# Kernel tuning notes

Hardware: AMD Instinct MI355X
Metric: run time of the kernel (lower is better)

Reference implementation:

```python
import jax, jax.numpy as jnp
import numpy as np

N, E, P = 50000, 800000, 12
C0, H1, H2 = 2, 32, 64


def gcn(x, W, b, src, dst, dinv):
    xw = x @ W                                   # [N, out]
    msg = (dinv[src] * dinv[dst])[:, None] * xw[src]
    agg = jax.ops.segment_sum(msg, dst, num_segments=x.shape[0])
    agg = agg + (dinv * dinv)[:, None] * xw      # self-loop term
    return agg + b


def tgcn_cell(x, H, W, b, Wl, bl, src, dst, dinv):
    # TGCN GRU cell (gates stacked as [z, r, h] along leading dim of W/b/Wl/bl)
    cz = gcn(x, W[0], b[0], src, dst, dinv)
    Z = jax.nn.sigmoid(jnp.concatenate([cz, H], axis=1) @ Wl[0] + bl[0])
    cr = gcn(x, W[1], b[1], src, dst, dinv)
    R = jax.nn.sigmoid(jnp.concatenate([cr, H], axis=1) @ Wl[1] + bl[1])
    ch = gcn(x, W[2], b[2], src, dst, dinv)
    Ht = jnp.tanh(jnp.concatenate([ch, H * R], axis=1) @ Wl[2] + bl[2])
    return Z * H + (1.0 - Z) * Ht


def a3tgcn(X, att, W, b, Wl, bl, src, dst, dinv):
    # X: [N, C, P]; attention-weighted sum of per-period TGCN outputs with H=0
    probs = jax.nn.softmax(att)
    n, out = X.shape[0], W.shape[2]
    H0 = jnp.zeros((n, out), X.dtype)

    def body(acc, inp):
        xp, p = inp
        return acc + p * tgcn_cell(xp, H0, W, b, Wl, bl, src, dst, dinv), None

    acc, _ = jax.lax.scan(body, jnp.zeros((n, out), X.dtype),
                          (jnp.moveaxis(X, 2, 0), probs))
    return acc


def setup_inputs() -> dict:
    key = jax.random.key(0)
    ks = jax.random.split(key, 16)
    s = 0.1
    return {
        "x_1": jax.random.normal(ks[0], (N, C0, P), jnp.float32),
        "edge_index_1": jax.random.randint(ks[1], (2, E), 0, N),
        "x_2": jax.random.normal(ks[2], (8, C0, P), jnp.float32),
        "edge_index_2": jax.random.randint(ks[3], (2, 8), 0, 8),
        # A3TGCN layer 1 (in=C0, out=H1): gates stacked [z, r, h]
        "W1": jax.random.normal(ks[4], (3, C0, H1), jnp.float32) * s,
        "b1": jnp.zeros((3, H1), jnp.float32),
        "Wl1": jax.random.normal(ks[5], (3, 2 * H1, H1), jnp.float32) * s,
        "bl1": jnp.zeros((3, H1), jnp.float32),
        "att1": jax.random.normal(ks[6], (P,), jnp.float32),
        # A3TGCN layer 2 (in=H1+1, out=H2)
        "W2": jax.random.normal(ks[7], (3, H1 + 1, H2), jnp.float32) * s,
        "b2": jnp.zeros((3, H2), jnp.float32),
        "Wl2": jax.random.normal(ks[8], (3, 2 * H2, H2), jnp.float32) * s,
        "bl2": jnp.zeros((3, H2), jnp.float32),
        "att2": jax.random.normal(ks[9], (P,), jnp.float32),
        # MLP head
        "lw1": jax.random.normal(ks[10], (H2, H1), jnp.float32) * s,
        "lb1": jnp.zeros((H1,), jnp.float32),
        "lw2": jax.random.normal(ks[11], (H1, P), jnp.float32) * s,
        "lb2": jnp.zeros((P,), jnp.float32),
    }


def reference(x_1, edge_index_1, x_2, edge_index_2,
              W1, b1, Wl1, bl1, att1,
              W2, b2, Wl2, bl2, att2,
              lw1, lb1, lw2, lb2):
    src, dst = edge_index_1[0], edge_index_1[1]
    n, periods = x_1.shape[0], x_1.shape[2]
    # degree (with self-loop) for symmetric GCN normalization
    deg = jax.ops.segment_sum(jnp.ones(src.shape[0], x_1.dtype), dst,
                              num_segments=n) + 1.0
    dinv = jax.lax.rsqrt(deg)

    time = x_1[:, -1, :]                                        # [N, P]
    h = jax.nn.relu(a3tgcn(x_1, att1, W1, b1, Wl1, bl1, src, dst, dinv))
    h = jnp.concatenate([jnp.repeat(h[:, :, None], periods, axis=2),
                         time[:, None, :]], axis=1)             # [N, H1+1, P]
    h = jax.nn.relu(a3tgcn(h, att2, W2, b2, Wl2, bl2, src, dst, dinv))
    h = jax.nn.relu(h @ lw1 + lb1)
    return h @ lw2 + lb2                                        # [N, P]
```

## Files before the change

kernel.cpp:

```cpp
#include <hip/hip_runtime.h>
#include <hip/hip_bf16.h>
#include <hip/hip_fp16.h>
#include <math.h>


typedef float f4v __attribute__((ext_vector_type(4)));

static __device__ __forceinline__ unsigned short f2bf(float f) {
    unsigned u = __float_as_uint(f);
    unsigned r = (u + 0x7FFFu + ((u >> 16) & 1u)) >> 16;
    return (unsigned short)r;
}
static __device__ __forceinline__ float bf2f(unsigned short u) {
    return __uint_as_float(((unsigned)u) << 16);
}
static __device__ __forceinline__ unsigned short f2h(float f) {
    __half h = __float2half_rn(f);
    return *reinterpret_cast<unsigned short*>(&h);
}
static __device__ __forceinline__ float h2f(unsigned short u) {
    __half h;
    *reinterpret_cast<unsigned short*>(&h) = u;
    return __half2float(h);
}

__global__ void zero_ints(int* __restrict__ a, int n) {
    int i = blockIdx.x * blockDim.x + threadIdx.x;
    if (i < n) a[i] = 0;
}

__global__ void cvt_count(const float* __restrict__ in, unsigned short* __restrict__ outh,
                          int n4, int ncb,
                          const int* __restrict__ dst, int* __restrict__ cnt,
                          int* __restrict__ epos, int E) {
    if ((int)blockIdx.x < ncb) {
        int i = (blockIdx.x * blockDim.x + threadIdx.x) * 4;
        if (i + 3 < n4) {
            f4v v = __builtin_nontemporal_load((const f4v*)(in + i));
            ushort4 u = make_ushort4(f2bf(v.x), f2bf(v.y), f2bf(v.z), f2bf(v.w));
            *(ushort4*)(outh + i) = u;
        } else {
            for (int k = 0; k < 4; ++k)
                if (i + k < n4) outh[i + k] = f2bf(in[i + k]);
        }
    } else {
        int e = (blockIdx.x - ncb) * blockDim.x + threadIdx.x;
        if (e < E) {
            int d = __builtin_nontemporal_load(dst + e);
            int pos = atomicAdd(&cnt[d], 1);
            __builtin_nontemporal_store(pos, epos + e);
        }
    }
}

__global__ __launch_bounds__(256) void scan_blocksum(
    const int* __restrict__ cnt, float* __restrict__ dinv,
    int* __restrict__ bsum, int n) {
    int base = blockIdx.x * 1024 + threadIdx.x * 4;
    int s = 0;
    if (base + 3 < n) {
        int4 v = *(const int4*)(cnt + base);
        dinv[base + 0] = rsqrtf((float)v.x + 1.f);
        dinv[base + 1] = rsqrtf((float)v.y + 1.f);
        dinv[base + 2] = rsqrtf((float)v.z + 1.f);
        dinv[base + 3] = rsqrtf((float)v.w + 1.f);
        s = v.x + v.y + v.z + v.w;
    } else {
        for (int k = 0; k < 4; ++k)
            if (base + k < n) {
                int v = cnt[base + k];
                dinv[base + k] = rsqrtf((float)v + 1.f);
                s += v;
            }
    }
    #pragma unroll
    for (int off = 32; off > 0; off >>= 1) s += __shfl_down(s, off, 64);
    __shared__ int ws[4];
    int lane = threadIdx.x & 63, wid = threadIdx.x >> 6;
    if (lane == 0) ws[wid] = s;
    __syncthreads();
    if (threadIdx.x == 0) bsum[blockIdx.x] = ws[0] + ws[1] + ws[2] + ws[3];
}

__global__ void scan_boffs(const int* __restrict__ bsum, int* __restrict__ boffs,
                           int* __restrict__ rowptr, int nb, int n) {
    int lane = threadIdx.x;
    int carry = 0;
    for (int base = 0; base < nb; base += 64) {
        int i = base + lane;
        int v = (i < nb) ? bsum[i] : 0;
        int orig = v;
        #pragma unroll
        for (int off = 1; off < 64; off <<= 1) {
            int t = __shfl_up(v, off, 64);
            if (lane >= off) v += t;
        }
        if (i < nb) boffs[i] = carry + v - orig;
        carry += __shfl(v, 63, 64);
    }
    if (lane == 0) rowptr[n] = carry;
}

__global__ __launch_bounds__(256) void scan_write(
    const int* __restrict__ cnt, const int* __restrict__ boffs,
    int* __restrict__ rowptr, int n) {
    int base = blockIdx.x * 1024 + threadIdx.x * 4;
    int4 v = make_int4(0, 0, 0, 0);
    if (base + 3 < n) {
        v = *(const int4*)(cnt + base);
    } else {
        if (base + 0 < n) v.x = cnt[base + 0];
        if (base + 1 < n) v.y = cnt[base + 1];
        if (base + 2 < n) v.z = cnt[base + 2];
        if (base + 3 < n) v.w = cnt[base + 3];
    }
    int t0 = v.x, t1 = t0 + v.y, t2 = t1 + v.z, t3 = t2 + v.w;
    int lane = threadIdx.x & 63, wid = threadIdx.x >> 6;
    int sc = t3;
    #pragma unroll
    for (int off = 1; off < 64; off <<= 1) {
        int t = __shfl_up(sc, off, 64);
        if (lane >= off) sc += t;
    }
    __shared__ int ws[4];
    if (lane == 63) ws[wid] = sc;
    __syncthreads();
    int woff = 0;
    for (int w = 0; w < wid; ++w) woff += ws[w];
    int off0 = boffs[blockIdx.x] + woff + sc - t3;
    if (base + 3 < n) {
        *(int4*)(rowptr + base) = make_int4(off0, off0 + t0, off0 + t1, off0 + t2);
    } else {
        if (base + 0 < n) rowptr[base + 0] = off0;
        if (base + 1 < n) rowptr[base + 1] = off0 + t0;
        if (base + 2 < n) rowptr[base + 2] = off0 + t1;
        if (base + 3 < n) rowptr[base + 3] = off0 + t2;
    }
}

__global__ void scatter_edges(const int* __restrict__ src, const int* __restrict__ dst,
                              const int* __restrict__ epos,
                              const float* __restrict__ dinv, const int* __restrict__ rowptr,
                              unsigned* __restrict__ cwp, int E) {
    int e = blockIdx.x * blockDim.x + threadIdx.x;
    if (e >= E) return;
    int s = __builtin_nontemporal_load(src + e);
    int d = __builtin_nontemporal_load(dst + e);
    int pos = __builtin_nontemporal_load(epos + e);
    int idx = rowptr[d] + pos;
    float w = dinv[s] * dinv[d];
    unsigned pk = (unsigned)(unsigned short)s | ((unsigned)f2h(w) << 16);
    __builtin_nontemporal_store(pk, cwp + idx);
}

__global__ __launch_bounds__(256) void prep_kernel(
    const float* __restrict__ W1, const float* __restrict__ b1,
    const float* __restrict__ Wl1, const float* __restrict__ bl1,
    const float* __restrict__ att1,
    const float* __restrict__ W2, const float* __restrict__ b2,
    const float* __restrict__ Wl2, const float* __restrict__ bl2,
    const float* __restrict__ att2, float* __restrict__ small) {
    int tid = threadIdx.x;
    for (int t = tid; t < 192; t += blockDim.x) {
        int which = t >> 5, hh = t & 31;
        int g = (which < 3) ? 0 : 2;
        int kind = which % 3;
        const float* Wl = Wl1 + g * 64 * 32;
        float s = 0.f;
        if (kind < 2) {
            const float* Wr = W1 + g * 2 * 32 + kind * 32;
            for (int k = 0; k < 32; ++k) s += Wr[k] * Wl[k * 32 + hh];
        } else {
            const float* br = b1 + g * 32;
            for (int k = 0; k < 32; ++k) s += br[k] * Wl[k * 32 + hh];
            s += bl1[g * 32 + hh];
        }
        small[t] = s;
    }
    for (int t = tid; t < 4096; t += blockDim.x) {
        int gg = t >> 11;
        int rem = t & 2047;
        int i = rem >> 6, j = rem & 63;
        int g = gg ? 2 : 0;
        const float* Wl = Wl2 + g * 128 * 64;
        const float* Wr = W2 + g * 33 * 64 + i * 64;
        float s = 0.f;
        for (int k = 0; k < 64; ++k) s += Wr[k] * Wl[k * 64 + j];
        small[256 + gg * 2048 + i * 64 + j] = s;
    }
    for (int t = tid; t < 256; t += blockDim.x) {
        int which = t >> 6, j = t & 63;
        int g = (which == 0 || which == 2) ? 0 : 2;
        const float* Wl = Wl2 + g * 128 * 64;
        float s = 0.f;
        if (which < 2) {
            const float* Wr = W2 + g * 33 * 64 + 32 * 64;
            for (int k = 0; k < 64; ++k) s += Wr[k] * Wl[k * 64 + j];
        } else {
            const float* br = b2 + g * 64;
            for (int k = 0; k < 64; ++k) s += br[k] * Wl[k * 64 + j];
            s += bl2[g * 64 + j];
        }
        small[4352 + which * 64 + j] = s;
    }
    if (tid == 0) {
        float mx = att1[0];
        for (int p = 1; p < 12; ++p) mx = fmaxf(mx, att1[p]);
        float e[12], sm = 0.f;
        for (int p = 0; p < 12; ++p) { e[p] = expf(att1[p] - mx); sm += e[p]; }
        for (int p = 0; p < 12; ++p) small[192 + p] = e[p] / sm;
        mx = att2[0];
        for (int p = 1; p < 12; ++p) mx = fmaxf(mx, att2[p]);
        sm = 0.f;
        for (int p = 0; p < 12; ++p) { e[p] = expf(att2[p] - mx); sm += e[p]; }
        for (int p = 0; p < 12; ++p) small[4608 + p] = e[p] / sm;
    }
}

__global__ __launch_bounds__(256) void agg1_layer1(
    const float* __restrict__ X, const unsigned short* __restrict__ Xh,
    const int* __restrict__ rowptr, const unsigned* __restrict__ cwp,
    const float* __restrict__ dinv, const float* __restrict__ small,
    unsigned short* __restrict__ hout, float* __restrict__ atime, int n) {
    int lane = threadIdx.x & 31;
    int node = (blockIdx.x * blockDim.x + threadIdx.x) >> 5;
    if (node >= n) return;
    int beg = rowptr[node], end = rowptr[node + 1];
    float acc = 0.f;
    if (lane < 24) {
        float dn = dinv[node];
        acc = dn * dn * __builtin_nontemporal_load(X + (size_t)node * 24 + lane);
        float a0 = 0.f, a1 = 0.f, a2 = 0.f, a3 = 0.f;
        int j = beg;
        for (; j + 4 <= end; j += 4) {
            unsigned c0 = __builtin_nontemporal_load(cwp + j);
            unsigned c1 = __builtin_nontemporal_load(cwp + j + 1);
            unsigned c2 = __builtin_nontemporal_load(cwp + j + 2);
            unsigned c3 = __builtin_nontemporal_load(cwp + j + 3);
            a0 = fmaf(h2f(c0 >> 16), bf2f(Xh[(c0 & 0xFFFFu) * 24 + lane]), a0);
            a1 = fmaf(h2f(c1 >> 16), bf2f(Xh[(c1 & 0xFFFFu) * 24 + lane]), a1);
            a2 = fmaf(h2f(c2 >> 16), bf2f(Xh[(c2 & 0xFFFFu) * 24 + lane]), a2);
            a3 = fmaf(h2f(c3 >> 16), bf2f(Xh[(c3 & 0xFFFFu) * 24 + lane]), a3);
        }
        for (; j < end; ++j) {
            unsigned c = __builtin_nontemporal_load(cwp + j);
            acc = fmaf(h2f(c >> 16), bf2f(Xh[(c & 0xFFFFu) * 24 + lane]), acc);
        }
        acc += (a0 + a1) + (a2 + a3);
    }
    if (lane >= 12 && lane < 24)
        __builtin_nontemporal_store(acc, atime + (size_t)node * 12 + lane - 12);
    float a0z = small[lane], a1z = small[32 + lane], c1z = small[64 + lane];
    float a0h = small[96 + lane], a1h = small[128 + lane], c1h = small[160 + lane];
    float hs = 0.f;
    #pragma unroll
    for (int p = 0; p < 12; ++p) {
        float x0 = __shfl(acc, p, 32);
        float x1 = __shfl(acc, 12 + p, 32);
        float z = 1.f / (1.f + __expf(-fmaf(x0, a0z, fmaf(x1, a1z, c1z))));
        float ht = tanhf(fmaf(x0, a0h, fmaf(x1, a1h, c1h)));
        hs = fmaf(small[192 + p] * (1.f - z), ht, hs);
    }
    hout[(size_t)node * 32 + lane] = f2bf(fmaxf(hs, 0.f));
}

__global__ __launch_bounds__(512, 8) void agg2_layer2(
    const unsigned short* __restrict__ hbuf, const float* __restrict__ atime,
    const int* __restrict__ rowptr, const unsigned* __restrict__ cwp,
    const float* __restrict__ dinv, const float* __restrict__ small,
    const float* __restrict__ lw1, const float* __restrict__ lb1,
    const float* __restrict__ lw2, const float* __restrict__ lb2,
    float* __restrict__ out, int n) {
    __shared__ __align__(16) float4 wqs[1024];
    __shared__ __align__(16) float s_lw1[2048];
    __shared__ float s_pr[16];
    __shared__ __align__(16) float4 scr[8][16];

    for (int t = threadIdx.x; t < 4096; t += 512) {
        int s = t & 3, j = (t >> 2) & 63, k2 = t >> 8;
        int k = 2 * k2 + (s >> 1), zh = s & 1;
        ((float*)wqs)[t] = small[256 + zh * 2048 + k * 64 + j];
    }
    for (int t = threadIdx.x; t < 2048; t += 512) s_lw1[t] = lw1[t];
    if (threadIdx.x < 16) s_pr[threadIdx.x] = (threadIdx.x < 12) ? small[4608 + threadIdx.x] : 0.f;
    __syncthreads();

    int lane = threadIdx.x & 63;
    int wid = threadIdx.x >> 6;
    int ch = lane & 31, half = lane >> 5;
    float qz = small[4352 + lane], qh = small[4416 + lane];
    float czv = small[4480 + lane], chv = small[4544 + lane];
    float lb1v = lb1[ch];
    int p_ = lane & 15, q_ = lane >> 4;
    float lb2v = (q_ == 0 && p_ < 12) ? lb2[p_] : 0.f;
    float wlw2[8];
    #pragma unroll
    for (int i = 0; i < 8; ++i)
        wlw2[i] = (p_ < 12) ? lw2[(q_ * 8 + i) * 12 + p_] : 0.f;

    int totalw = gridDim.x * 8;
    for (int node = blockIdx.x * 8 + wid; node < n; node += totalw) {
        int beg = rowptr[node], end = rowptr[node + 1];
        float dn = dinv[node];
        float acc = (half == 0) ? dn * dn * bf2f(hbuf[(size_t)node * 32 + ch]) : 0.f;
        float a1 = 0.f, a2 = 0.f, a3 = 0.f;
        int j = beg + half;
        for (; j + 6 < end; j += 8) {
            unsigned c0 = __builtin_nontemporal_load(cwp + j);
            unsigned c1 = __builtin_nontemporal_load(cwp + j + 2);
            unsigned c2 = __builtin_nontemporal_load(cwp + j + 4);
            unsigned c3 = __builtin_nontemporal_load(cwp + j + 6);
            acc = fmaf(h2f(c0 >> 16), bf2f(hbuf[(size_t)(c0 & 0xFFFFu) * 32 + ch]), acc);
            a1  = fmaf(h2f(c1 >> 16), bf2f(hbuf[(size_t)(c1 & 0xFFFFu) * 32 + ch]), a1);
            a2  = fmaf(h2f(c2 >> 16), bf2f(hbuf[(size_t)(c2 & 0xFFFFu) * 32 + ch]), a2);
            a3  = fmaf(h2f(c3 >> 16), bf2f(hbuf[(size_t)(c3 & 0xFFFFu) * 32 + ch]), a3);
        }
        for (; j < end; j += 2) {
            unsigned c = __builtin_nontemporal_load(cwp + j);
            acc = fmaf(h2f(c >> 16), bf2f(hbuf[(size_t)(c & 0xFFFFu) * 32 + ch]), acc);
        }
        acc += (a1 + a2) + a3;
        acc += __shfl_xor(acc, 32, 64);

        if (half == 0) ((float*)&scr[wid][0])[ch] = acc;
        asm volatile("s_waitcnt lgkmcnt(0)" ::: "memory");

        float p0z = czv, p0h = chv;
        const float4* arow = &scr[wid][0];
        #pragma unroll
        for (int c = 0; c < 8; ++c) {
            float4 av = arow[c];
            float4 w0 = wqs[(2 * c) * 64 + lane];
            float4 w1 = wqs[(2 * c + 1) * 64 + lane];
            p0z = fmaf(av.x, w0.x, p0z); p0h = fmaf(av.x, w0.y, p0h);
            p0z = fmaf(av.y, w0.z, p0z); p0h = fmaf(av.y, w0.w, p0h);
            p0z = fmaf(av.z, w1.x, p0z); p0h = fmaf(av.z, w1.y, p0h);
            p0z = fmaf(av.w, w1.z, p0z); p0h = fmaf(av.w, w1.w, p0h);
        }
        const f4v* trow = (const f4v*)(atime + (size_t)node * 12);
        f4v tA = __builtin_nontemporal_load(trow);
        f4v tB = __builtin_nontemporal_load(trow + 1);
        f4v tC = __builtin_nontemporal_load(trow + 2);
        float tt[12] = {tA.x, tA.y, tA.z, tA.w, tB.x, tB.y, tB.z, tB.w,
                        tC.x, tC.y, tC.z, tC.w};
        float acc2 = 0.f;
        #pragma unroll
        for (int p = 0; p < 12; ++p) {
            float t = tt[p];
            float ez = __expf(-fmaf(t, qz, p0z));
            float eh = __expf(-2.f * fmaf(t, qh, p0h));
            float R = __builtin_amdgcn_rcpf((1.f + ez) * (1.f + eh));
            acc2 = fmaf(s_pr[p] * ez * (1.f - eh), R, acc2);
        }
        float h2 = fmaxf(acc2, 0.f);
        ((float*)&scr[wid][0])[lane] = h2;
        asm volatile("s_waitcnt lgkmcnt(0)" ::: "memory");

        float h3 = half ? 0.f : lb1v;
        const float4* hrow = &scr[wid][half * 8];
        #pragma unroll
        for (int c = 0; c < 8; ++c) {
            float4 hv = hrow[c];
            int jb = half * 32 + c * 4;
            h3 = fmaf(hv.x, s_lw1[(jb + 0) * 32 + ch], h3);
            h3 = fmaf(hv.y, s_lw1[(jb + 1) * 32 + ch], h3);
            h3 = fmaf(hv.z, s_lw1[(jb + 2) * 32 + ch], h3);
            h3 = fmaf(hv.w, s_lw1[(jb + 3) * 32 + ch], h3);
        }
        h3 += __shfl_xor(h3, 32, 64);
        h3 = fmaxf(h3, 0.f);

        float o = lb2v;
        #pragma unroll
        for (int i = 0; i < 8; ++i) {
            float h3k = __shfl(h3, q_ * 8 + i, 64);
            o = fmaf(h3k, wlw2[i], o);
        }
        o += __shfl_xor(o, 16, 64);
        o += __shfl_xor(o, 32, 64);
        if (lane < 12)
            __builtin_nontemporal_store(o, out + (size_t)node * 12 + lane);
    }
}

extern "C" void kernel_launch(void* const* d_in, const int* in_sizes, int n_in,
                              void* d_out, int out_size, void* d_ws, size_t ws_size,
                              hipStream_t stream) {
    const float* x1   = (const float*)d_in[0];
    const int*   eidx = (const int*)d_in[1];
    const float* W1   = (const float*)d_in[4];
    const float* b1   = (const float*)d_in[5];
    const float* Wl1  = (const float*)d_in[6];
    const float* bl1  = (const float*)d_in[7];
    const float* att1 = (const float*)d_in[8];
    const float* W2   = (const float*)d_in[9];
    const float* b2   = (const float*)d_in[10];
    const float* Wl2  = (const float*)d_in[11];
    const float* bl2  = (const float*)d_in[12];
    const float* att2 = (const float*)d_in[13];
    const float* lw1  = (const float*)d_in[14];
    const float* lb1  = (const float*)d_in[15];
    const float* lw2  = (const float*)d_in[16];
    const float* lb2  = (const float*)d_in[17];
    (void)n_in; (void)out_size; (void)ws_size;

    int N = in_sizes[0] / 24;
    int E = in_sizes[1] / 2;
    const int* srcp = eidx;
    const int* dstp = eidx + E;
    int nb = (N + 1023) / 1024;
    int ncvt = N * 24;
    int ncb = (ncvt / 4 + 255) / 256;
    int neb = (E + 255) / 256;

    char* ws = (char*)d_ws;
    size_t off = 0;
    auto alloc = [&](size_t bytes) -> char* {
        char* p = ws + off;
        off += (bytes + 511) & ~(size_t)511;
        return p;
    };
    int*            cnt    = (int*)alloc((size_t)N * 4);
    int*            rowptr = (int*)alloc((size_t)(N + 1) * 4);
    float*          dinv   = (float*)alloc((size_t)N * 4);
    int*            epos   = (int*)alloc((size_t)E * 4);
    unsigned*       cwp    = (unsigned*)alloc((size_t)E * 4);
    unsigned short* x1h    = (unsigned short*)alloc((size_t)N * 24 * 2);
    unsigned short* hbuf   = (unsigned short*)alloc((size_t)N * 32 * 2);
    float*          atime  = (float*)alloc((size_t)N * 12 * 4);
    float*          small  = (float*)alloc(4624 * 4);
    int*            bsum   = (int*)alloc((size_t)nb * 4);
    int*            boffs  = (int*)alloc((size_t)nb * 4);

    prep_kernel<<<1, 256, 0, stream>>>(W1, b1, Wl1, bl1, att1, W2, b2, Wl2, bl2, att2, small);
    zero_ints<<<(N + 255) / 256, 256, 0, stream>>>(cnt, N);
    cvt_count<<<ncb + neb, 256, 0, stream>>>(x1, x1h, ncvt, ncb, dstp, cnt, epos, E);
    scan_blocksum<<<nb, 256, 0, stream>>>(cnt, dinv, bsum, N);
    scan_boffs<<<1, 64, 0, stream>>>(bsum, boffs, rowptr, nb, N);
    scan_write<<<nb, 256, 0, stream>>>(cnt, boffs, rowptr, N);
    scatter_edges<<<neb, 256, 0, stream>>>(srcp, dstp, epos, dinv, rowptr, cwp, E);
    agg1_layer1<<<(N * 32 + 255) / 256, 256, 0, stream>>>(x1, x1h, rowptr, cwp, dinv, small, hbuf, atime, N);
    agg2_layer2<<<1024, 512, 0, stream>>>(hbuf, atime, rowptr, cwp, dinv, small,
                                          lw1, lb1, lw2, lb2, (float*)d_out, N);
}
```

Measured before the change: 181.1 us.

## Pad bf16 features to 32, store time in bf16, memset counts, double grid

The bf16 copy of the input features is padded from 24 to 32 channels per node, so each gathered row is 64-byte aligned during aggregation. The per-node time aggregate is stored in bf16 instead of fp32, and the layer-2 kernel loads it at the top of the node loop so the load overlaps the edge gather. The zeroing kernel is replaced by hipMemsetAsync, and the layer-2 grid grows from 1024 to 2048 blocks. The trade-offs are more conversion work for the padding, a larger padded buffer, and reduced precision on the time channel.

```diff
diff --git a/kernel.cpp b/kernel.cpp
--- a/kernel.cpp
+++ b/kernel.cpp
@@ -5,6 +5,7 @@
 
 
 typedef float f4v __attribute__((ext_vector_type(4)));
+typedef unsigned u2v __attribute__((ext_vector_type(2)));
 
 static __device__ __forceinline__ unsigned short f2bf(float f) {
     unsigned u = __float_as_uint(f);
@@ -24,24 +25,21 @@
     return __half2float(h);
 }
 
-__global__ void zero_ints(int* __restrict__ a, int n) {
-    int i = blockIdx.x * blockDim.x + threadIdx.x;
-    if (i < n) a[i] = 0;
-}
-
 __global__ void cvt_count(const float* __restrict__ in, unsigned short* __restrict__ outh,
-                          int n4, int ncb,
+                          int n32, int ncb,
                           const int* __restrict__ dst, int* __restrict__ cnt,
                           int* __restrict__ epos, int E) {
     if ((int)blockIdx.x < ncb) {
         int i = (blockIdx.x * blockDim.x + threadIdx.x) * 4;
-        if (i + 3 < n4) {
-            f4v v = __builtin_nontemporal_load((const f4v*)(in + i));
-            ushort4 u = make_ushort4(f2bf(v.x), f2bf(v.y), f2bf(v.z), f2bf(v.w));
+        if (i < n32) {
+            int node = i >> 5, c = i & 31;
+            const float* row = in + (size_t)node * 24;
+            ushort4 u;
+            u.x = (c + 0 < 24) ? f2bf(__builtin_nontemporal_load(row + c + 0)) : (unsigned short)0;
+            u.y = (c + 1 < 24) ? f2bf(__builtin_nontemporal_load(row + c + 1)) : (unsigned short)0;
+            u.z = (c + 2 < 24) ? f2bf(__builtin_nontemporal_load(row + c + 2)) : (unsigned short)0;
+            u.w = (c + 3 < 24) ? f2bf(__builtin_nontemporal_load(row + c + 3)) : (unsigned short)0;
             *(ushort4*)(outh + i) = u;
-        } else {
-            for (int k = 0; k < 4; ++k)
-                if (i + k < n4) outh[i + k] = f2bf(in[i + k]);
         }
     } else {
         int e = (blockIdx.x - ncb) * blockDim.x + threadIdx.x;
@@ -221,7 +219,7 @@
     const float* __restrict__ X, const unsigned short* __restrict__ Xh,
     const int* __restrict__ rowptr, const unsigned* __restrict__ cwp,
     const float* __restrict__ dinv, const float* __restrict__ small,
-    unsigned short* __restrict__ hout, float* __restrict__ atime, int n) {
+    unsigned short* __restrict__ hout, unsigned short* __restrict__ atimeh, int n) {
     int lane = threadIdx.x & 31;
     int node = (blockIdx.x * blockDim.x + threadIdx.x) >> 5;
     if (node >= n) return;
@@ -237,19 +235,19 @@
             unsigned c1 = __builtin_nontemporal_load(cwp + j + 1);
             unsigned c2 = __builtin_nontemporal_load(cwp + j + 2);
             unsigned c3 = __builtin_nontemporal_load(cwp + j + 3);
-            a0 = fmaf(h2f(c0 >> 16), bf2f(Xh[(c0 & 0xFFFFu) * 24 + lane]), a0);
-            a1 = fmaf(h2f(c1 >> 16), bf2f(Xh[(c1 & 0xFFFFu) * 24 + lane]), a1);
-            a2 = fmaf(h2f(c2 >> 16), bf2f(Xh[(c2 & 0xFFFFu) * 24 + lane]), a2);
-            a3 = fmaf(h2f(c3 >> 16), bf2f(Xh[(c3 & 0xFFFFu) * 24 + lane]), a3);
+            a0 = fmaf(h2f(c0 >> 16), bf2f(Xh[(c0 & 0xFFFFu) * 32 + lane]), a0);
+            a1 = fmaf(h2f(c1 >> 16), bf2f(Xh[(c1 & 0xFFFFu) * 32 + lane]), a1);
+            a2 = fmaf(h2f(c2 >> 16), bf2f(Xh[(c2 & 0xFFFFu) * 32 + lane]), a2);
+            a3 = fmaf(h2f(c3 >> 16), bf2f(Xh[(c3 & 0xFFFFu) * 32 + lane]), a3);
         }
         for (; j < end; ++j) {
             unsigned c = __builtin_nontemporal_load(cwp + j);
-            acc = fmaf(h2f(c >> 16), bf2f(Xh[(c & 0xFFFFu) * 24 + lane]), acc);
+            acc = fmaf(h2f(c >> 16), bf2f(Xh[(c & 0xFFFFu) * 32 + lane]), acc);
         }
         acc += (a0 + a1) + (a2 + a3);
     }
     if (lane >= 12 && lane < 24)
-        __builtin_nontemporal_store(acc, atime + (size_t)node * 12 + lane - 12);
+        atimeh[(size_t)node * 12 + lane - 12] = f2bf(acc);
     float a0z = small[lane], a1z = small[32 + lane], c1z = small[64 + lane];
     float a0h = small[96 + lane], a1h = small[128 + lane], c1h = small[160 + lane];
     float hs = 0.f;
@@ -265,7 +263,7 @@
 }
 
 __global__ __launch_bounds__(512, 8) void agg2_layer2(
-    const unsigned short* __restrict__ hbuf, const float* __restrict__ atime,
+    const unsigned short* __restrict__ hbuf, const unsigned short* __restrict__ atimeh,
     const int* __restrict__ rowptr, const unsigned* __restrict__ cwp,
     const float* __restrict__ dinv, const float* __restrict__ small,
     const float* __restrict__ lw1, const float* __restrict__ lb1,
@@ -300,6 +298,11 @@
 
     int totalw = gridDim.x * 8;
     for (int node = blockIdx.x * 8 + wid; node < n; node += totalw) {
+        const u2v* trow = (const u2v*)(atimeh + (size_t)node * 12);
+        u2v tA = __builtin_nontemporal_load(trow);
+        u2v tB = __builtin_nontemporal_load(trow + 1);
+        u2v tC = __builtin_nontemporal_load(trow + 2);
+
         int beg = rowptr[node], end = rowptr[node + 1];
         float dn = dinv[node];
         float acc = (half == 0) ? dn * dn * bf2f(hbuf[(size_t)node * 32 + ch]) : 0.f;
@@ -337,12 +340,12 @@
             p0z = fmaf(av.z, w1.x, p0z); p0h = fmaf(av.z, w1.y, p0h);
             p0z = fmaf(av.w, w1.z, p0z); p0h = fmaf(av.w, w1.w, p0h);
         }
-        const f4v* trow = (const f4v*)(atime + (size_t)node * 12);
-        f4v tA = __builtin_nontemporal_load(trow);
-        f4v tB = __builtin_nontemporal_load(trow + 1);
-        f4v tC = __builtin_nontemporal_load(trow + 2);
-        float tt[12] = {tA.x, tA.y, tA.z, tA.w, tB.x, tB.y, tB.z, tB.w,
-                        tC.x, tC.y, tC.z, tC.w};
+        float tt[12] = {bf2f((unsigned short)(tA.x & 0xFFFFu)), bf2f((unsigned short)(tA.x >> 16)),
+                        bf2f((unsigned short)(tA.y & 0xFFFFu)), bf2f((unsigned short)(tA.y >> 16)),
+                        bf2f((unsigned short)(tB.x & 0xFFFFu)), bf2f((unsigned short)(tB.x >> 16)),
+                        bf2f((unsigned short)(tB.y & 0xFFFFu)), bf2f((unsigned short)(tB.y >> 16)),
+                        bf2f((unsigned short)(tC.x & 0xFFFFu)), bf2f((unsigned short)(tC.x >> 16)),
+                        bf2f((unsigned short)(tC.y & 0xFFFFu)), bf2f((unsigned short)(tC.y >> 16))};
         float acc2 = 0.f;
         #pragma unroll
         for (int p = 0; p < 12; ++p) {
@@ -409,8 +412,8 @@
     const int* srcp = eidx;
     const int* dstp = eidx + E;
     int nb = (N + 1023) / 1024;
-    int ncvt = N * 24;
-    int ncb = (ncvt / 4 + 255) / 256;
+    int n32 = N * 32;
+    int ncb = (n32 / 4 + 255) / 256;
     int neb = (E + 255) / 256;
 
     char* ws = (char*)d_ws;
@@ -425,21 +428,21 @@
     float*          dinv   = (float*)alloc((size_t)N * 4);
     int*            epos   = (int*)alloc((size_t)E * 4);
     unsigned*       cwp    = (unsigned*)alloc((size_t)E * 4);
-    unsigned short* x1h    = (unsigned short*)alloc((size_t)N * 24 * 2);
+    unsigned short* x1h    = (unsigned short*)alloc((size_t)n32 * 2);
     unsigned short* hbuf   = (unsigned short*)alloc((size_t)N * 32 * 2);
-    float*          atime  = (float*)alloc((size_t)N * 12 * 4);
+    unsigned short* atimeh = (unsigned short*)alloc((size_t)N * 12 * 2);
     float*          small  = (float*)alloc(4624 * 4);
     int*            bsum   = (int*)alloc((size_t)nb * 4);
     int*            boffs  = (int*)alloc((size_t)nb * 4);
 
+    (void)hipMemsetAsync(cnt, 0, (size_t)N * 4, stream);
     prep_kernel<<<1, 256, 0, stream>>>(W1, b1, Wl1, bl1, att1, W2, b2, Wl2, bl2, att2, small);
-    zero_ints<<<(N + 255) / 256, 256, 0, stream>>>(cnt, N);
-    cvt_count<<<ncb + neb, 256, 0, stream>>>(x1, x1h, ncvt, ncb, dstp, cnt, epos, E);
+    cvt_count<<<ncb + neb, 256, 0, stream>>>(x1, x1h, n32, ncb, dstp, cnt, epos, E);
     scan_blocksum<<<nb, 256, 0, stream>>>(cnt, dinv, bsum, N);
     scan_boffs<<<1, 64, 0, stream>>>(bsum, boffs, rowptr, nb, N);
     scan_write<<<nb, 256, 0, stream>>>(cnt, boffs, rowptr, N);
     scatter_edges<<<neb, 256, 0, stream>>>(srcp, dstp, epos, dinv, rowptr, cwp, E);
-    agg1_layer1<<<(N * 32 + 255) / 256, 256, 0, stream>>>(x1, x1h, rowptr, cwp, dinv, small, hbuf, atime, N);
-    agg2_layer2<<<1024, 512, 0, stream>>>(hbuf, atime, rowptr, cwp, dinv, small,
+    agg1_layer1<<<(N * 32 + 255) / 256, 256, 0, stream>>>(x1, x1h, rowptr, cwp, dinv, small, hbuf, atimeh, N);
+    agg2_layer2<<<2048, 512, 0, stream>>>(hbuf, atimeh, rowptr, cwp, dinv, small,
                                           lw1, lb1, lw2, lb2, (float*)d_out, N);
 }
```

Result: slower. 196.5 us (+8.5%).
